# Kernel optimization log

Hardware: AMD Instinct MI355X
Metric: run time of the kernel (lower is better)

The kernel has to match this reference:

```python
import jax, jax.numpy as jnp
import numpy as np
from jax import lax

T = 8192
D_MODEL = 768
D_RNN = 1024
KW = 4  # conv kernel width


def setup_inputs() -> dict:
    key = jax.random.key(0)
    ks = jax.random.split(key, 9)
    x = jax.random.normal(ks[0], (T, D_MODEL), jnp.float32)
    # equinox nn.Linear(in, out): weight [out, in], bias [out]
    w1 = jax.random.normal(ks[1], (2 * D_RNN, D_MODEL), jnp.float32) / np.sqrt(D_MODEL)
    b1 = jnp.zeros((2 * D_RNN,), jnp.float32)
    # nn.Conv1d(d_rnn, d_rnn, 4, use_bias=False): kernel [out_ch, in_ch, kw]
    conv_w = jax.random.normal(ks[2], (D_RNN, D_RNN, KW), jnp.float32) / np.sqrt(D_RNN * KW)
    w_rg = jax.random.normal(ks[3], (2 * D_RNN, D_RNN), jnp.float32) / np.sqrt(D_RNN)
    b_rg = jnp.zeros((2 * D_RNN,), jnp.float32)
    w_out = jax.random.normal(ks[4], (D_MODEL, D_RNN), jnp.float32) / np.sqrt(D_RNN)
    b_out = jnp.zeros((D_MODEL,), jnp.float32)
    # Lambda ~ U(inv_sigmoid(0.9)^{1/8}, inv_sigmoid(0.999)^{1/8}) as in __init__
    inv_sig = lambda p: np.log(1.0 / (1.0 - p))
    lower = np.power(inv_sig(0.9), 1.0 / 8.0)
    upper = np.power(inv_sig(0.999), 1.0 / 8.0)
    Lambda = jax.random.uniform(ks[5], (D_RNN,), jnp.float32, lower, upper)
    return {"x": x, "w1": w1, "b1": b1, "conv_w": conv_w, "w_rg": w_rg,
            "b_rg": b_rg, "w_out": w_out, "b_out": b_out, "Lambda": Lambda}


def _rglru_forward(x, w1, b1, conv_w, w_rg, b_rg, w_out, b_out, Lambda):
    # lin1 then split into gate branch (gelu) and recurrent branch
    h = x @ w1.T + b1                       # [T, 2*D_RNN]
    a_branch = jax.nn.gelu(h[:, :D_RNN])    # [T, D_RNN]
    b_branch = h[:, D_RNN:]                 # [T, D_RNN]
    # causal conv1d: lhs [N=1, C, T], rhs [O, I, KW], left pad 3
    bc = lax.conv_general_dilated(b_branch.T[None], conv_w, (1,), [(KW - 1, 0)])[0].T  # [T, D_RNN]
    # RG-LRU gating
    g = jax.nn.sigmoid(bc @ w_rg.T + b_rg)  # [T, 2*D_RNN]
    inp_gate = g[:, :D_RNN]
    rec_gate = g[:, D_RNN:]
    a_t = jnp.exp(-8.0 * jax.nn.softplus(Lambda)[None, :] * rec_gate)  # [T, D_RNN]
    gated_x = jnp.sqrt(1.0 - a_t ** 2) * inp_gate * bc

    def rec_step(state, xs):
        gx, av = xs
        hn = av * state + gx
        return hn, hn

    _, y = lax.scan(rec_step, jnp.zeros((D_RNN,), x.dtype), (gated_x, a_t))
    return (a_branch * y) @ w_out.T + b_out  # [T, D_MODEL]


def reference(x, w1, b1, conv_w, w_rg, b_rg, w_out, b_out, Lambda):
    return _rglru_forward(x, w1, b1, conv_w, w_rg, b_rg, w_out, b_out, Lambda)
```

## Files before the change

### kernel.cpp

```cpp
#include <hip/hip_runtime.h>
#include <hip/hip_bf16.h>
#include <stdint.h>


#define T_LEN 8192
#define DM 768
#define DR 1024
#define NC 128
#define CL 64

typedef __bf16 bf16x8 __attribute__((ext_vector_type(8)));
typedef float  f32x4  __attribute__((ext_vector_type(4)));

#define AS1 __attribute__((address_space(1)))
#define AS3 __attribute__((address_space(3)))

__device__ __forceinline__ void cp16_g2l(const void* g, void* l) {
    __builtin_amdgcn_global_load_lds((const AS1 void*)g, (AS3 void*)l, 16, 0, 0);
}

__device__ __forceinline__ float gelu_tanh(float x) {
    const float inner = 0.7978845608028654f * (x + 0.044715f * x * x * x);
    return 0.5f * x * (1.f + tanhf(inner));
}

__device__ __forceinline__ __bf16 f2b(float v) {
    __hip_bfloat16 h = __float2bfloat16(v);
    return *reinterpret_cast<__bf16*>(&h);
}

template<int BN, int EPI, bool SHIFT>
__global__ __launch_bounds__(256, 4)
void gemm_mfma(const __hip_bfloat16* __restrict__ A,
               const __hip_bfloat16* __restrict__ B,
               const float* __restrict__ bias,
               void* __restrict__ Cv,
               int K, int lda, int N,
               __hip_bfloat16* __restrict__ D2)
{
    constexpr int NI  = BN / 32;
    constexpr int BLD = (BN * 4) / 256;
    constexpr int NLD = 2 + BLD;
    __shared__ __align__(16) unsigned char smem[32768];
    __bf16* Asb = (__bf16*)smem;
    __bf16* Bsb = (__bf16*)(smem + 16384);

    const int tid  = threadIdx.x;
    const int lane = tid & 63;
    const int wave = tid >> 6;
    const size_t m0 = (size_t)blockIdx.x * 128;
    const int    n0 = blockIdx.y * BN;
    const int wm = (wave >> 1) * 64;
    const int wn = (wave & 1) * (BN / 2);

    f32x4 acc[4][NI];
#pragma unroll
    for (int i = 0; i < 4; ++i)
#pragma unroll
        for (int j = 0; j < NI; ++j)
            acc[i][j] = f32x4{0.f, 0.f, 0.f, 0.f};

    const int frow = lane & 15;
    const int fq   = lane >> 4;

    auto stage = [&](int buf, int k0) {
#pragma unroll
        for (int q = 0; q < 2; ++q) {
            const int lin = q * 256 + tid;
            const int rr  = lin >> 2;
            const int gc  = (lin & 3) ^ ((rr >> 1) & 3);
            const size_t ar = m0 + rr + (SHIFT ? (size_t)(k0 >> 10) : 0);
            const int    ac = SHIFT ? (k0 & 1023) : k0;
            cp16_g2l(A + ar * (size_t)lda + ac + gc * 8, Asb + buf * 4096 + lin * 8);
        }
#pragma unroll
        for (int q = 0; q < BLD; ++q) {
            const int lin = q * 256 + tid;
            const int rr  = lin >> 2;
            const int gc  = (lin & 3) ^ ((rr >> 1) & 3);
            cp16_g2l(B + (size_t)(n0 + rr) * K + k0 + gc * 8,
                     Bsb + buf * (BN * 32) + lin * 8);
        }
    };

    const int nt = K / 32;
    stage(0, 0);
    int cur = 0;
    for (int t = 0; t < nt; ++t) {
        if (t + 1 < nt) {
            stage(cur ^ 1, (t + 1) * 32);
            asm volatile("s_waitcnt vmcnt(%0)" :: "n"(NLD) : "memory");
        } else {
            asm volatile("s_waitcnt vmcnt(0)" ::: "memory");
        }
        __builtin_amdgcn_sched_barrier(0);
        __builtin_amdgcn_s_barrier();
        __builtin_amdgcn_sched_barrier(0);

        bf16x8 af[4], bfr[NI];
#pragma unroll
        for (int mi = 0; mi < 4; ++mi) {
            const int R = wm + mi * 16 + frow;
            af[mi] = *(const bf16x8*)&Asb[cur * 4096 + R * 32 + ((fq ^ ((R >> 1) & 3)) * 8)];
        }
#pragma unroll
        for (int ni = 0; ni < NI; ++ni) {
            const int R = wn + ni * 16 + frow;
            bfr[ni] = *(const bf16x8*)&Bsb[cur * (BN * 32) + R * 32 + ((fq ^ ((R >> 1) & 3)) * 8)];
        }
        asm volatile("s_waitcnt lgkmcnt(0)" ::: "memory");
        __builtin_amdgcn_sched_barrier(0);
        __builtin_amdgcn_s_barrier();
        __builtin_amdgcn_sched_barrier(0);

        __builtin_amdgcn_s_setprio(1);
#pragma unroll
        for (int mi = 0; mi < 4; ++mi)
#pragma unroll
            for (int ni = 0; ni < NI; ++ni)
                acc[mi][ni] = __builtin_amdgcn_mfma_f32_16x16x32_bf16(
                    af[mi], bfr[ni], acc[mi][ni], 0, 0, 0);
        __builtin_amdgcn_s_setprio(0);
        cur ^= 1;
    }

    __syncthreads();
    const int er = fq * 4;
    const int ec = frow;

    if (EPI == 0) {
        float* Cl = (float*)smem;
#pragma unroll
        for (int ni = 0; ni < NI; ++ni) {
            const int cc = wn + ni * 16 + ec;
            const float bv = bias ? bias[n0 + cc] : 0.f;
#pragma unroll
            for (int mi = 0; mi < 4; ++mi)
#pragma unroll
                for (int r2 = 0; r2 < 4; ++r2) {
                    const int R = wm + mi * 16 + er + r2;
                    Cl[R * 64 + ((((cc >> 2) ^ (R & 7)) << 2) | (cc & 3))] =
                        acc[mi][ni][r2] + bv;
                }
        }
        __syncthreads();
        float* outp = (float*)Cv;
#pragma unroll
        for (int p = 0; p < 8; ++p) {
            const int R   = (tid >> 4) + p * 16;
            const int chn = tid & 15;
            const f32x4 v = *(const f32x4*)&Cl[R * 64 + ((chn ^ (R & 7)) << 2)];
            *(f32x4*)&outp[(m0 + R) * (size_t)N + n0 + chn * 4] = v;
        }
    } else {
        __bf16* Cl = (__bf16*)smem;
        const bool ahalf = (EPI == 2) && (n0 < 1024);
#pragma unroll
        for (int ni = 0; ni < NI; ++ni) {
            const int cc = wn + ni * 16 + ec;
            const float bv = bias ? bias[n0 + cc] : 0.f;
#pragma unroll
            for (int mi = 0; mi < 4; ++mi)
#pragma unroll
                for (int r2 = 0; r2 < 4; ++r2) {
                    const int R = wm + mi * 16 + er + r2;
                    float v = acc[mi][ni][r2] + bv;
                    if (EPI == 2 && ahalf) v = gelu_tanh(v);
                    Cl[R * 128 + ((((cc >> 3) ^ (R & 7)) << 3) | (cc & 7))] = f2b(v);
                }
        }
        __syncthreads();
#pragma unroll
        for (int p = 0; p < 8; ++p) {
            const int R   = (tid >> 4) + p * 16;
            const int chn = tid & 15;
            const bf16x8 v = *(const bf16x8*)&Cl[R * 128 + ((chn ^ (R & 7)) << 3)];
            if (EPI == 1) {
                *(bf16x8*)((__bf16*)Cv + (m0 + R) * (size_t)N + n0 + chn * 8) = v;
            } else if (n0 < 1024) {
                *(bf16x8*)((__bf16*)Cv + (m0 + R) * 1024 + n0 + chn * 8) = v;
            } else {
                *(bf16x8*)((__bf16*)D2 + (m0 + R + 3) * 1024 + (n0 - 1024) + chn * 8) = v;
            }
        }
    }
}

__global__ __launch_bounds__(256, 2)
void conv_mfma(const __hip_bfloat16* __restrict__ bbp,
               const __hip_bfloat16* __restrict__ W,
               __hip_bfloat16* __restrict__ C)
{
    __shared__ __align__(16) unsigned char smem[73984];
    __bf16* Ah = (__bf16*)smem;
    __bf16* Bt = (__bf16*)(smem + 8448);

    const int tid  = threadIdx.x;
    const int lane = tid & 63;
    const int wave = tid >> 6;
    const size_t m0 = (size_t)blockIdx.x * 128;
    const int    n0 = blockIdx.y * 128;
    const int wm = (wave >> 1) * 64;
    const int wn = (wave & 1) * 64;

    f32x4 acc[4][4];
#pragma unroll
    for (int i = 0; i < 4; ++i)
#pragma unroll
        for (int j = 0; j < 4; ++j)
            acc[i][j] = f32x4{0.f, 0.f, 0.f, 0.f};

    const int frow = lane & 15;
    const int fq   = lane >> 4;

    auto stageA = [&](int kc) {
#pragma unroll
        for (int q = 0; q < 2; ++q) {
            const int lin = q * 256 + tid;
            const int rr  = lin >> 2;
            const int gc  = (lin & 3) ^ ((rr >> 1) & 3);
            cp16_g2l(bbp + (m0 + rr) * 1024 + kc + gc * 8, Ah + lin * 8);
        }
        if (tid < 16) {
            const int lin = 512 + tid;
            const int rr  = lin >> 2;
            const int gc  = (lin & 3) ^ ((rr >> 1) & 3);
            cp16_g2l(bbp + (m0 + rr) * 1024 + kc + gc * 8, Ah + lin * 8);
        }
    };
    auto stageB = [&](int buf, int kc) {
#pragma unroll
        for (int s = 0; s < 4; ++s)
#pragma unroll
            for (int q = 0; q < 2; ++q) {
                const int lin = q * 256 + tid;
                const int rr  = lin >> 2;
                const int gc  = (lin & 3) ^ ((rr >> 1) & 3);
                cp16_g2l(W + (size_t)(n0 + rr) * 4096 + s * 1024 + kc + gc * 8,
                         Bt + buf * 16384 + s * 4096 + lin * 8);
            }
    };

    stageA(0);
    stageB(0, 0);
    int bcur = 0;
    for (int t = 0; t < 32; ++t) {
        if (t + 1 < 32) {
            stageB(bcur ^ 1, (t + 1) * 32);
            asm volatile("s_waitcnt vmcnt(8)" ::: "memory");
        } else {
            asm volatile("s_waitcnt vmcnt(0)" ::: "memory");
        }
        __builtin_amdgcn_sched_barrier(0);
        __builtin_amdgcn_s_barrier();
        __builtin_amdgcn_sched_barrier(0);

        __builtin_amdgcn_s_setprio(1);
#pragma unroll
        for (int s = 0; s < 4; ++s) {
            bf16x8 af[4], bfr[4];
#pragma unroll
            for (int mi = 0; mi < 4; ++mi) {
                const int R = wm + mi * 16 + frow + s;
                af[mi] = *(const bf16x8*)&Ah[R * 32 + ((fq ^ ((R >> 1) & 3)) * 8)];
            }
#pragma unroll
            for (int ni = 0; ni < 4; ++ni) {
                const int R = wn + ni * 16 + frow;
                bfr[ni] = *(const bf16x8*)&Bt[bcur * 16384 + s * 4096 + R * 32 +
                                              ((fq ^ ((R >> 1) & 3)) * 8)];
            }
#pragma unroll
            for (int mi = 0; mi < 4; ++mi)
#pragma unroll
                for (int ni = 0; ni < 4; ++ni)
                    acc[mi][ni] = __builtin_amdgcn_mfma_f32_16x16x32_bf16(
                        af[mi], bfr[ni], acc[mi][ni], 0, 0, 0);
        }
        __builtin_amdgcn_s_setprio(0);
        __builtin_amdgcn_sched_barrier(0);
        __builtin_amdgcn_s_barrier();
        __builtin_amdgcn_sched_barrier(0);
        if (t + 1 < 32) stageA((t + 1) * 32);
        bcur ^= 1;
    }

    __syncthreads();
    const int er = fq * 4;
    const int ec = frow;
    __bf16* Cl = (__bf16*)smem;
#pragma unroll
    for (int ni = 0; ni < 4; ++ni) {
        const int cc = wn + ni * 16 + ec;
#pragma unroll
        for (int mi = 0; mi < 4; ++mi)
#pragma unroll
            for (int r2 = 0; r2 < 4; ++r2) {
                const int R = wm + mi * 16 + er + r2;
                Cl[R * 128 + ((((cc >> 3) ^ (R & 7)) << 3) | (cc & 7))] =
                    f2b(acc[mi][ni][r2]);
            }
    }
    __syncthreads();
#pragma unroll
    for (int p = 0; p < 8; ++p) {
        const int R   = (tid >> 4) + p * 16;
        const int chn = tid & 15;
        const bf16x8 v = *(const bf16x8*)&Cl[R * 128 + ((chn ^ (R & 7)) << 3)];
        *(bf16x8*)((__bf16*)C + (m0 + R) * 1024 + n0 + chn * 8) = v;
    }
}

#define PREP_X   6291456
#define PREP_W1  (PREP_X + 1572864)
#define PREP_WRG (PREP_W1 + 2097152)
#define PREP_WO  (PREP_WRG + 786432)
#define PREP_CW  (PREP_WO + 4194304)
#define PREP_TOT (PREP_CW + 3072)
__global__ void prep_kernel(const float* __restrict__ x, const float* __restrict__ w1,
                            const float* __restrict__ w_rg, const float* __restrict__ w_out,
                            const float* __restrict__ conv_w,
                            __hip_bfloat16* __restrict__ xb, __hip_bfloat16* __restrict__ w1b,
                            __hip_bfloat16* __restrict__ w_rgb, __hip_bfloat16* __restrict__ w_outb,
                            __hip_bfloat16* __restrict__ wbigb, __hip_bfloat16* __restrict__ bbp)
{
    const int idx = blockIdx.x * 256 + threadIdx.x;
    if (idx < PREP_X) {
        xb[idx] = __float2bfloat16(x[idx]);
    } else if (idx < PREP_W1) {
        const int i = idx - PREP_X;  w1b[i] = __float2bfloat16(w1[i]);
    } else if (idx < PREP_WRG) {
        const int i = idx - PREP_W1; w_rgb[i] = __float2bfloat16(w_rg[i]);
    } else if (idx < PREP_WO) {
        const int i = idx - PREP_WRG; w_outb[i] = __float2bfloat16(w_out[i]);
    } else if (idx < PREP_CW) {
        const int n = idx - PREP_WO;
        const int o = n >> 12, r = n & 4095, k = r >> 10, i = r & 1023;
        wbigb[n] = __float2bfloat16(conv_w[o * 4096 + i * 4 + k]);
    } else {
        bbp[idx - PREP_CW] = __float2bfloat16(0.f);
    }
}

__global__ void scan_pass1(const __hip_bfloat16* __restrict__ gp,
                           const __hip_bfloat16* __restrict__ bc,
                           const float* __restrict__ Lambda,
                           float* __restrict__ ch, float* __restrict__ ca)
{
    const int c = blockIdx.y * 256 + threadIdx.x;
    const int j = blockIdx.x;
    const float cl = -8.f * log1pf(expf(Lambda[c]));
    float h = 0.f, ap = 1.f;
    const int t0 = j * CL;
    for (int tt = 0; tt < CL; ++tt) {
        const int t = t0 + tt;
        const long gi = (long)t * 2048 + c;
        const float ig = 1.f / (1.f + expf(-__bfloat162float(gp[gi])));
        const float rg = 1.f / (1.f + expf(-__bfloat162float(gp[gi + 1024])));
        const float a  = expf(cl * rg);
        const float gx = sqrtf(fmaxf(0.f, 1.f - a * a)) * ig *
                         __bfloat162float(bc[(long)t * 1024 + c]);
        h  = fmaf(a, h, gx);
        ap *= a;
    }
    ch[j * 1024 + c] = h;
    ca[j * 1024 + c] = ap;
}

__global__ void scan_combine(float* __restrict__ ch, const float* __restrict__ ca)
{
    const int c = blockIdx.x * 256 + threadIdx.x;
    float carry = 0.f;
    for (int j = 0; j < NC; ++j) {
        const float hj = ch[j * 1024 + c];
        const float aj = ca[j * 1024 + c];
        ch[j * 1024 + c] = carry;
        carry = fmaf(aj, carry, hj);
    }
}

__global__ void scan_pass2(const __hip_bfloat16* __restrict__ gp, const __hip_bfloat16* bc,
                           const float* __restrict__ Lambda,
                           const float* __restrict__ carry_in,
                           const __hip_bfloat16* __restrict__ ab,
                           __hip_bfloat16* zb)
{
    const int c = blockIdx.y * 256 + threadIdx.x;
    const int j = blockIdx.x;
    const float cl = -8.f * log1pf(expf(Lambda[c]));
    float h = carry_in[j * 1024 + c];
    const int t0 = j * CL;
    for (int tt = 0; tt < CL; ++tt) {
        const int t = t0 + tt;
        const long gi = (long)t * 2048 + c;
        const long bi = (long)t * 1024 + c;
        const float ig = 1.f / (1.f + expf(-__bfloat162float(gp[gi])));
        const float rg = 1.f / (1.f + expf(-__bfloat162float(gp[gi + 1024])));
        const float a  = expf(cl * rg);
        const float gx = sqrtf(fmaxf(0.f, 1.f - a * a)) * ig * __bfloat162float(bc[bi]);
        h = fmaf(a, h, gx);
        zb[bi] = __float2bfloat16(__bfloat162float(ab[bi]) * h);
    }
}

extern "C" void kernel_launch(void* const* d_in, const int* in_sizes, int n_in,
                              void* d_out, int out_size, void* d_ws, size_t ws_size,
                              hipStream_t stream)
{
    const float* x      = (const float*)d_in[0];
    const float* w1     = (const float*)d_in[1];
    const float* b1     = (const float*)d_in[2];
    const float* conv_w = (const float*)d_in[3];
    const float* w_rg   = (const float*)d_in[4];
    const float* b_rg   = (const float*)d_in[5];
    const float* w_out  = (const float*)d_in[6];
    const float* b_out  = (const float*)d_in[7];
    const float* Lambda = (const float*)d_in[8];
    float* out = (float*)d_out;
    (void)in_sizes; (void)n_in; (void)out_size; (void)ws_size;

    char* p = (char*)d_ws;
    auto alloc = [&](size_t bytes) { char* r = p; p += (bytes + 255) & ~255ULL; return r; };
    __hip_bfloat16* gpre  = (__hip_bfloat16*)alloc(8192ULL * 2048 * 2);
    __hip_bfloat16* ab    = (__hip_bfloat16*)alloc(8192ULL * 1024 * 2);
    __hip_bfloat16* bbp   = (__hip_bfloat16*)alloc(8200ULL * 1024 * 2);
    __hip_bfloat16* bcb   = (__hip_bfloat16*)alloc(8192ULL * 1024 * 2);
    __hip_bfloat16* wbigb = (__hip_bfloat16*)alloc(1024ULL * 4096 * 2);
    __hip_bfloat16* xb    = (__hip_bfloat16*)alloc(8192ULL * 768 * 2);
    __hip_bfloat16* w1b   = (__hip_bfloat16*)alloc(2048ULL * 768 * 2);
    __hip_bfloat16* w_rgb = (__hip_bfloat16*)alloc(2048ULL * 1024 * 2);
    __hip_bfloat16* w_outb= (__hip_bfloat16*)alloc(768ULL * 1024 * 2);
    float*          chv   = (float*)alloc(NC * 1024ULL * 4);
    float*          cav   = (float*)alloc(NC * 1024ULL * 4);
    __hip_bfloat16* zb    = bcb;

    prep_kernel<<<PREP_TOT / 256, 256, 0, stream>>>(x, w1, w_rg, w_out, conv_w,
                                                    xb, w1b, w_rgb, w_outb, wbigb, bbp);

    {
        dim3 grid(T_LEN / 128, 2048 / 128);
        gemm_mfma<128, 2, false><<<grid, 256, 0, stream>>>(xb, w1b, b1, ab, DM, DM, 2048, bbp);
    }

    {
        dim3 grid(T_LEN / 128, 1024 / 128);
        conv_mfma<<<grid, 256, 0, stream>>>(bbp, wbigb, bcb);
    }

    {
        dim3 grid(T_LEN / 128, 2048 / 128);
        gemm_mfma<128, 1, false><<<grid, 256, 0, stream>>>(bcb, w_rgb, b_rg, gpre, DR, DR, 2048, nullptr);
    }

    {
        dim3 gs(NC, DR / 256);
        scan_pass1<<<gs, 256, 0, stream>>>(gpre, bcb, Lambda, chv, cav);
        scan_combine<<<DR / 256, 256, 0, stream>>>(chv, cav);
        scan_pass2<<<gs, 256, 0, stream>>>(gpre, bcb, Lambda, chv, ab, zb);
    }

    {
        dim3 grid(T_LEN / 128, DM / 64);
        gemm_mfma<64, 0, false><<<grid, 256, 0, stream>>>(zb, w_outb, b_out, out, DR, DR, DM, nullptr);
    }
}
```

Before: 272.3 us.

## Load conv weights directly into registers in MFMA fragment layout, double-buffer A in LDS

The prep kernel now writes the conv weights pre-permuted into the exact per-lane MFMA B-fragment order. The conv GEMM loads them straight from global memory into registers, double-buffered across iterations, instead of staging them through LDS. LDS usage drops from about 74KB to 32KB, and A is now double-buffered. This cuts LDS traffic and may allow more occupancy, at the cost of more VGPRs and uncoalesced-but-contiguous global loads of weights that each block repeats.

```diff
diff --git a/kernel.cpp b/kernel.cpp
--- a/kernel.cpp
+++ b/kernel.cpp
@@ -188,12 +188,11 @@
 
 __global__ __launch_bounds__(256, 2)
 void conv_mfma(const __hip_bfloat16* __restrict__ bbp,
-               const __hip_bfloat16* __restrict__ W,
+               const __hip_bfloat16* __restrict__ WB,
                __hip_bfloat16* __restrict__ C)
 {
-    __shared__ __align__(16) unsigned char smem[73984];
+    __shared__ __align__(16) unsigned char smem[32768];
     __bf16* Ah = (__bf16*)smem;
-    __bf16* Bt = (__bf16*)(smem + 8448);
 
     const int tid  = threadIdx.x;
     const int lane = tid & 63;
@@ -213,41 +212,41 @@
     const int frow = lane & 15;
     const int fq   = lane >> 4;
 
-    auto stageA = [&](int kc) {
+    const __bf16* wbase = (const __bf16*)WB +
+        ((size_t)((n0 + wn) >> 4) << 16) + (lane << 3);
+
+    auto loadB = [&](bf16x8 (&b)[4][4], int t1) {
+#pragma unroll
+        for (int s = 0; s < 4; ++s)
+#pragma unroll
+            for (int ni = 0; ni < 4; ++ni)
+                b[s][ni] = *(const bf16x8*)(wbase + ((size_t)ni << 16) +
+                                            t1 * 2048 + s * 512);
+    };
+    auto stageA = [&](int abuf, int kc) {
 #pragma unroll
         for (int q = 0; q < 2; ++q) {
             const int lin = q * 256 + tid;
             const int rr  = lin >> 2;
             const int gc  = (lin & 3) ^ ((rr >> 1) & 3);
-            cp16_g2l(bbp + (m0 + rr) * 1024 + kc + gc * 8, Ah + lin * 8);
+            cp16_g2l(bbp + (m0 + rr) * 1024 + kc + gc * 8, Ah + abuf * 4224 + lin * 8);
         }
         if (tid < 16) {
             const int lin = 512 + tid;
             const int rr  = lin >> 2;
             const int gc  = (lin & 3) ^ ((rr >> 1) & 3);
-            cp16_g2l(bbp + (m0 + rr) * 1024 + kc + gc * 8, Ah + lin * 8);
+            cp16_g2l(bbp + (m0 + rr) * 1024 + kc + gc * 8, Ah + abuf * 4224 + lin * 8);
         }
     };
-    auto stageB = [&](int buf, int kc) {
-#pragma unroll
-        for (int s = 0; s < 4; ++s)
-#pragma unroll
-            for (int q = 0; q < 2; ++q) {
-                const int lin = q * 256 + tid;
-                const int rr  = lin >> 2;
-                const int gc  = (lin & 3) ^ ((rr >> 1) & 3);
-                cp16_g2l(W + (size_t)(n0 + rr) * 4096 + s * 1024 + kc + gc * 8,
-                         Bt + buf * 16384 + s * 4096 + lin * 8);
-            }
-    };
-
-    stageA(0);
-    stageB(0, 0);
-    int bcur = 0;
-    for (int t = 0; t < 32; ++t) {
+
+    bf16x8 bA[4][4], bB[4][4];
+    stageA(0, 0);
+    loadB(bA, 0);
+
+    auto iter = [&](bf16x8 (&bCur)[4][4], bf16x8 (&bNxt)[4][4], int t) {
         if (t + 1 < 32) {
-            stageB(bcur ^ 1, (t + 1) * 32);
-            asm volatile("s_waitcnt vmcnt(8)" ::: "memory");
+            loadB(bNxt, t + 1);
+            asm volatile("s_waitcnt vmcnt(16)" ::: "memory");
         } else {
             asm volatile("s_waitcnt vmcnt(0)" ::: "memory");
         }
@@ -255,34 +254,34 @@
         __builtin_amdgcn_s_barrier();
         __builtin_amdgcn_sched_barrier(0);
 
+        const int ab = (t & 1) * 4224;
         __builtin_amdgcn_s_setprio(1);
 #pragma unroll
         for (int s = 0; s < 4; ++s) {
-            bf16x8 af[4], bfr[4];
+            bf16x8 af[4];
 #pragma unroll
             for (int mi = 0; mi < 4; ++mi) {
                 const int R = wm + mi * 16 + frow + s;
-                af[mi] = *(const bf16x8*)&Ah[R * 32 + ((fq ^ ((R >> 1) & 3)) * 8)];
-            }
-#pragma unroll
-            for (int ni = 0; ni < 4; ++ni) {
-                const int R = wn + ni * 16 + frow;
-                bfr[ni] = *(const bf16x8*)&Bt[bcur * 16384 + s * 4096 + R * 32 +
-                                              ((fq ^ ((R >> 1) & 3)) * 8)];
+                af[mi] = *(const bf16x8*)&Ah[ab + R * 32 + ((fq ^ ((R >> 1) & 3)) * 8)];
             }
 #pragma unroll
             for (int mi = 0; mi < 4; ++mi)
 #pragma unroll
                 for (int ni = 0; ni < 4; ++ni)
                     acc[mi][ni] = __builtin_amdgcn_mfma_f32_16x16x32_bf16(
-                        af[mi], bfr[ni], acc[mi][ni], 0, 0, 0);
+                        af[mi], bCur[s][ni], acc[mi][ni], 0, 0, 0);
         }
         __builtin_amdgcn_s_setprio(0);
         __builtin_amdgcn_sched_barrier(0);
         __builtin_amdgcn_s_barrier();
         __builtin_amdgcn_sched_barrier(0);
-        if (t + 1 < 32) stageA((t + 1) * 32);
-        bcur ^= 1;
+        if (t + 1 < 32) stageA((t + 1) & 1, (t + 1) * 32);
+    };
+
+#pragma unroll 1
+    for (int tp = 0; tp < 16; ++tp) {
+        iter(bA, bB, 2 * tp);
+        iter(bB, bA, 2 * tp + 1);
     }
 
     __syncthreads();
@@ -334,9 +333,19 @@
     } else if (idx < PREP_WO) {
         const int i = idx - PREP_WRG; w_outb[i] = __float2bfloat16(w_out[i]);
     } else if (idx < PREP_CW) {
-        const int n = idx - PREP_WO;
-        const int o = n >> 12, r = n & 4095, k = r >> 10, i = r & 1023;
-        wbigb[n] = __float2bfloat16(conv_w[o * 4096 + i * 4 + k]);
+        const int n    = idx - PREP_WO;
+        const int nt   = n >> 16;
+        const int r1   = n & 65535;
+        const int kcI  = r1 >> 11;
+        const int r2   = r1 & 2047;
+        const int s    = r2 >> 9;
+        const int r3   = r2 & 511;
+        const int l    = r3 >> 3;
+        const int j0   = r3 & 7;
+        const int frow = l & 15, fq = l >> 4;
+        const int o = nt * 16 + frow;
+        const int i = kcI * 32 + fq * 8 + j0;
+        wbigb[n] = __float2bfloat16(conv_w[o * 4096 + i * 4 + s]);
     } else {
         bbp[idx - PREP_CW] = __float2bfloat16(0.f);
     }
```

New measurement: 268.1 us. No clear change (-1.6%).
